# Kernel tuning notes

Measured on AMD Instinct MI355X. Metric: run time of the kernel, lower is better.

Reference implementation:

```python
import jax, jax.numpy as jnp
import numpy as np

B, S, D = 8, 512, 384
VOCAB = 50257


def setup_inputs() -> dict:
    key = jax.random.key(0)
    ks = jax.random.split(key, 8)
    tokens = jax.random.randint(ks[0], (B, S), 0, VOCAB)
    dep_types = jax.random.randint(ks[1], (B, S), 0, 64)
    dep_heads = jax.random.randint(ks[2], (B, S), 0, S)
    tok_table = jax.random.normal(ks[3], (VOCAB, D), dtype=jnp.float32) * 0.02
    # composition bilinear: out[o] = x1 @ Wc[o] @ x2 + bc[o]
    Wc = jax.random.normal(ks[4], (D, D, D), dtype=jnp.float32) * (1.0 / np.sqrt(D))
    bc = jax.random.normal(ks[5], (D,), dtype=jnp.float32) * 0.01
    # reduction Linear(seq_len, 1): weight (1, S), bias (1,)
    Wr = jax.random.normal(ks[6], (1, S), dtype=jnp.float32) * (1.0 / np.sqrt(S))
    br = jax.random.normal(ks[7], (1,), dtype=jnp.float32) * 0.01
    return {"tokens": tokens, "dep_types": dep_types, "dep_heads": dep_heads,
            "tok_table": tok_table, "Wc": Wc, "bc": bc, "Wr": Wr, "br": br}


def _composition_block(tok, heads, Wc, bc, Wr, br):
    # Original math (with the dep_transform-overwrite bug preserved):
    #   dep = tanh(tok)                                   [B,S,D]
    #   expanded[b,s1,s2,:] = tok[b,s2,:]
    #   masked_dep[b,s1,s2,:] = dep[b,s2,:] * (heads[b,s2]==s1)
    #   comp[b,s1,s2,o] = tanh(bilinear(tok[b,s2], masked_dep[b,s1,s2]))[o]
    #   y[b,s1,o] = sum_s2 Wr[0,s2]*comp[b,s1,s2,o] + br[0]
    # Since masked_dep is zero unless heads[b,s2]==s1, bilinear reduces to
    # bias-only (t_off) off-tree and full value (t_on) on-tree -> O(S) scatter.
    dep = jnp.tanh(tok)
    u = jnp.einsum('bsd,ode,bse->bso', tok, Wc, dep)      # [B,S,D] full bilinear value
    t_on = jnp.tanh(u + bc)                               # [B,S,D]
    t_off = jnp.tanh(bc)                                  # [D]
    w = Wr[0]                                             # [S]
    base = t_off * jnp.sum(w) + br[0]                     # [D]
    contrib = (t_on - t_off) * w[None, :, None]           # [B,S,D]
    scat = jax.vmap(lambda h, c: jnp.zeros((S, D), dtype=tok.dtype).at[h].add(c))(heads, contrib)
    return scat + base[None, None, :]                     # [B,S,D]


def reference(tokens, dep_types, dep_heads, tok_table, Wc, bc, Wr, br):
    depth = 1
    tok = tok_table[tokens]                               # [B,S,D]
    # dep_types embedding is computed in the original but its result is
    # discarded inside the block (bug); it does not affect the output.
    for _ in range(depth):
        tok = _composition_block(tok, dep_heads, Wc, bc, Wr, br)
    out_mask = (dep_heads == 0)[:, :, None]               # [B,S,1]
    return tok * out_mask.astype(tok.dtype)
```

## Files before the change

kernel.cpp:

```cpp
#include <hip/hip_runtime.h>

#define BB 8
#define SS 512
#define DD 384
#define K2 (DD * DD)
#define LCH 16
#define OT 4
#define KCH 8
#define NT 256
#define GROUPS (K2 / 4)
#define GPC (GROUPS / KCH)
#define ITERS (GPC / NT)
#define MAXL_CAP 1024

#define WS_LIST_OFF 16
#define WS_U_OFF 16400

__global__ void flag_kernel(const int* __restrict__ heads, int* __restrict__ countp,
                            int* __restrict__ list, int maxl) {
    int b = blockIdx.x;
    int s2 = threadIdx.x;
    int h = heads[b * SS + s2];
    if (heads[b * SS + h] == 0) {
        int idx = atomicAdd(countp, 1);
        if (idx < maxl) list[idx] = b * SS + s2;
    }
}

template <int HALF>
__device__ __forceinline__ void fold_step(float* red, int lane) {
#pragma unroll
    for (int i = 0; i < HALF; ++i) {
        float lo = red[i], hi = red[i + HALF];
        float send = (lane & HALF) ? lo : hi;
        float recv = __shfl_xor(send, HALF, 64);
        red[i] = (lane & HALF) ? (hi + recv) : (lo + recv);
    }
}

__global__ __launch_bounds__(NT, 3) void bilinear_kernel(
    const float* __restrict__ Wc, const float* __restrict__ tok_table,
    const int* __restrict__ tokens, const int* __restrict__ list,
    const int* __restrict__ countp, float* __restrict__ u, int maxl) {
    __shared__ alignas(16) float tokS[LCH][DD];
    __shared__ alignas(16) float depS[LCH][DD];

    const int tid = threadIdx.x;
    const int lane = tid & 63;
    const int wid = tid >> 6;
    const int o0 = blockIdx.x * OT;
    const int g0 = blockIdx.y * GPC;

    int total = *countp;
    if (total > maxl) total = maxl;

    for (int cb = 0; cb < total; cb += LCH) {
        for (int idx = tid; idx < LCH * DD; idx += NT) {
            int l = idx / DD;
            int i = idx - l * DD;
            float t = 0.f;
            if (cb + l < total) {
                int pos = list[cb + l];
                t = tok_table[(size_t)tokens[pos] * DD + i];
            }
            tokS[l][i] = t;
            depS[l][i] = tanhf(t);
        }
        __syncthreads();

        const int lmax = total - cb;

        float acc[LCH][OT];
#pragma unroll
        for (int l = 0; l < LCH; ++l)
#pragma unroll
            for (int j = 0; j < OT; ++j) acc[l][j] = 0.f;

        const float* wbase = Wc + (size_t)o0 * K2;
        float4 wv[OT], nv[OT];
        {
            const float* wp = wbase + 4 * (size_t)(g0 + tid);
#pragma unroll
            for (int r = 0; r < OT; ++r) wv[r] = *(const float4*)(wp + (size_t)r * K2);
        }

#pragma unroll 1
        for (int it = 0; it < ITERS; ++it) {
            int gc = g0 + it * NT + tid;

#pragma unroll
            for (int r = 0; r < OT; ++r) nv[r] = make_float4(0.f, 0.f, 0.f, 0.f);
            if (it + 1 < ITERS) {
                const float* wp = wbase + 4 * (size_t)(gc + NT);
#pragma unroll
                for (int r = 0; r < OT; ++r) nv[r] = *(const float4*)(wp + (size_t)r * K2);
            }

            int d = gc / 96;
            int e4 = gc - d * 96;

#pragma unroll
            for (int l4 = 0; l4 < LCH / 4; ++l4) {
                if (l4 * 4 < lmax) {
#pragma unroll
                    for (int li = 0; li < 4; ++li) {
                        const int l = l4 * 4 + li;
                        float td = tokS[l][d];
                        float4 dv = *(const float4*)(&depS[l][e4 * 4]);
                        float px = td * dv.x, py = td * dv.y;
                        float pz = td * dv.z, pw = td * dv.w;
#pragma unroll
                        for (int r = 0; r < OT; ++r)
                            acc[l][r] += px * wv[r].x + py * wv[r].y +
                                         pz * wv[r].z + pw * wv[r].w;
                    }
                }
            }
#pragma unroll
            for (int r = 0; r < OT; ++r) wv[r] = nv[r];
        }

        float red[LCH * OT];
#pragma unroll
        for (int k = 0; k < LCH * OT; ++k) red[k] = acc[k >> 2][k & 3];
        fold_step<32>(red, lane);
        fold_step<16>(red, lane);
        fold_step<8>(red, lane);
        fold_step<4>(red, lane);
        fold_step<2>(red, lane);
        fold_step<1>(red, lane);

        __syncthreads();
        float* redS = &tokS[0][0];
        redS[wid * 64 + lane] = red[0];
        __syncthreads();
        if (tid < 64) {
            int l = tid >> 2, j = tid & 3;
            if (l < lmax) {
                float s = redS[tid] + redS[64 + tid] + redS[128 + tid] + redS[192 + tid];
                atomicAdd(&u[(size_t)(cb + l) * DD + o0 + j], s);
            }
        }
        __syncthreads();
    }
}

__global__ __launch_bounds__(SS) void finalize_kernel(
    const int* __restrict__ heads, const float* __restrict__ Wr,
    const float* __restrict__ bc, const float* __restrict__ br,
    const int* __restrict__ list, const int* __restrict__ countp,
    const float* __restrict__ u, float* __restrict__ out, int maxl) {
    int b = blockIdx.x;
    int tid = threadIdx.x;

    __shared__ float wpart[SS / 64];
    __shared__ int hitlist[64];
    __shared__ int nh;
    if (tid == 0) nh = 0;
    __syncthreads();

    float w = Wr[tid];
#pragma unroll
    for (int off = 32; off > 0; off >>= 1) w += __shfl_down(w, off, 64);
    if ((tid & 63) == 0) wpart[tid >> 6] = w;

    if (heads[b * SS + tid] == 0) {
        int i = atomicAdd(&nh, 1);
        if (i < 64) hitlist[i] = tid;
    }
    __syncthreads();

    float sumw = 0.f;
#pragma unroll
    for (int q = 0; q < SS / 64; ++q) sumw += wpart[q];
    float brv = br[0];

    int total = *countp;
    if (total > maxl) total = maxl;
    int hn = nh;
    if (hn > 64) hn = 64;

    for (int i = 0; i < hn; ++i) {
        int s1 = hitlist[i];
        if (tid < DD) {
            int o = tid;
            float bco = bc[o];
            float t_off = tanhf(bco);
            float val = t_off * sumw + brv;
            for (int l = 0; l < total; ++l) {
                int pos = list[l];
                if ((pos >> 9) == b && heads[pos] == s1)
                    val += (tanhf(u[(size_t)l * DD + o] + bco) - t_off) * Wr[pos & 511];
            }
            out[(size_t)(b * SS + s1) * DD + o] = val;
        }
    }
}

extern "C" void kernel_launch(void* const* d_in, const int* in_sizes, int n_in,
                              void* d_out, int out_size, void* d_ws, size_t ws_size,
                              hipStream_t stream) {
    const int* tokens = (const int*)d_in[0];
    const int* heads = (const int*)d_in[2];
    const float* tok_table = (const float*)d_in[3];
    const float* Wc = (const float*)d_in[4];
    const float* bc = (const float*)d_in[5];
    const float* Wr = (const float*)d_in[6];
    const float* br = (const float*)d_in[7];
    float* out = (float*)d_out;

    char* ws = (char*)d_ws;
    int* countp = (int*)ws;
    int* list = (int*)(ws + WS_LIST_OFF);
    float* u = (float*)(ws + WS_U_OFF);

    long maxl_l = ((long)ws_size - WS_U_OFF) / (DD * 4);
    int maxl = maxl_l < 0 ? 0 : (maxl_l > MAXL_CAP ? MAXL_CAP : (int)maxl_l);

    hipMemsetAsync(d_ws, 0, (size_t)WS_U_OFF + (size_t)maxl * DD * 4, stream);
    hipMemsetAsync(d_out, 0, (size_t)out_size, stream);

    flag_kernel<<<BB, SS, 0, stream>>>(heads, countp, list, maxl);
    bilinear_kernel<<<dim3(DD / OT, KCH), NT, 0, stream>>>(
        Wc, tok_table, tokens, list, countp, u, maxl);
    finalize_kernel<<<BB, SS, 0, stream>>>(
        heads, Wr, bc, br, list, countp, u, out, maxl);
}
```

Baseline: 373.2 us.

## Precompute gathered token/tanh rows once and replace atomics with per-chunk partials

A single-block prep kernel now builds the list of active positions and writes gathered token embeddings and their tanh into workspace once. The bilinear blocks then only copy these rows with float4 loads instead of each redoing the gather and tanh. The atomic accumulation into u becomes plain stores of per-K-chunk partials, which finalize sums. This also removes the workspace memset and makes the weight prefetch unconditional. The trade-offs are a serial single-block prep stage and more workspace.

```diff
diff --git a/kernel.cpp b/kernel.cpp
--- a/kernel.cpp
+++ b/kernel.cpp
@@ -3,6 +3,7 @@
 #define BB 8
 #define SS 512
 #define DD 384
+#define D4 (DD / 4)
 #define K2 (DD * DD)
 #define LCH 16
 #define OT 4
@@ -12,18 +13,42 @@
 #define GPC (GROUPS / KCH)
 #define ITERS (GPC / NT)
 #define MAXL_CAP 1024
+#define PREP_NT 1024
 
 #define WS_LIST_OFF 16
-#define WS_U_OFF 16400
-
-__global__ void flag_kernel(const int* __restrict__ heads, int* __restrict__ countp,
-                            int* __restrict__ list, int maxl) {
-    int b = blockIdx.x;
-    int s2 = threadIdx.x;
-    int h = heads[b * SS + s2];
-    if (heads[b * SS + h] == 0) {
-        int idx = atomicAdd(countp, 1);
-        if (idx < maxl) list[idx] = b * SS + s2;
+#define WS_TOKW_OFF (WS_LIST_OFF + 4 * MAXL_CAP)
+
+__global__ __launch_bounds__(PREP_NT) void prep_kernel(
+    const int* __restrict__ heads, const int* __restrict__ tokens,
+    const float* __restrict__ tok_table, int* __restrict__ countp,
+    int* __restrict__ list, float* __restrict__ tokW, float* __restrict__ depW,
+    int maxl) {
+    __shared__ int cnt;
+    __shared__ int lst[MAXL_CAP];
+    const int tid = threadIdx.x;
+    if (tid == 0) cnt = 0;
+    __syncthreads();
+
+    for (int pos = tid; pos < BB * SS; pos += PREP_NT) {
+        int h = heads[pos];
+        if (heads[(pos & ~(SS - 1)) + h] == 0) {
+            int i = atomicAdd(&cnt, 1);
+            if (i < maxl) lst[i] = pos;
+        }
+    }
+    __syncthreads();
+
+    int total = cnt;
+    if (total > maxl) total = maxl;
+    if (tid == 0) *countp = total;
+    for (int i = tid; i < total; i += PREP_NT) list[i] = lst[i];
+
+    for (int idx = tid; idx < total * DD; idx += PREP_NT) {
+        int l = idx / DD;
+        int i = idx - l * DD;
+        float t = tok_table[(size_t)tokens[lst[l]] * DD + i];
+        tokW[idx] = t;
+        depW[idx] = tanhf(t);
     }
 }
 
@@ -39,9 +64,9 @@
 }
 
 __global__ __launch_bounds__(NT, 3) void bilinear_kernel(
-    const float* __restrict__ Wc, const float* __restrict__ tok_table,
-    const int* __restrict__ tokens, const int* __restrict__ list,
-    const int* __restrict__ countp, float* __restrict__ u, int maxl) {
+    const float* __restrict__ Wc, const float* __restrict__ tokW,
+    const float* __restrict__ depW, const int* __restrict__ countp,
+    float* __restrict__ u, int maxl) {
     __shared__ alignas(16) float tokS[LCH][DD];
     __shared__ alignas(16) float depS[LCH][DD];
 
@@ -55,16 +80,19 @@
     if (total > maxl) total = maxl;
 
     for (int cb = 0; cb < total; cb += LCH) {
-        for (int idx = tid; idx < LCH * DD; idx += NT) {
-            int l = idx / DD;
-            int i = idx - l * DD;
-            float t = 0.f;
-            if (cb + l < total) {
-                int pos = list[cb + l];
-                t = tok_table[(size_t)tokens[pos] * DD + i];
-            }
-            tokS[l][i] = t;
-            depS[l][i] = tanhf(t);
+        {
+            const float4* tw = (const float4*)tokW;
+            const float4* dw = (const float4*)depW;
+            float4* ts = (float4*)&tokS[0][0];
+            float4* ds = (float4*)&depS[0][0];
+            const float4 z = make_float4(0.f, 0.f, 0.f, 0.f);
+            for (int idx = tid; idx < LCH * D4; idx += NT) {
+                int l = idx / D4;
+                bool live = (cb + l) < total;
+                int src = cb * D4 + idx;
+                ts[idx] = live ? tw[src] : z;
+                ds[idx] = live ? dw[src] : z;
+            }
         }
         __syncthreads();
 
@@ -88,10 +116,9 @@
         for (int it = 0; it < ITERS; ++it) {
             int gc = g0 + it * NT + tid;
 
-#pragma unroll
-            for (int r = 0; r < OT; ++r) nv[r] = make_float4(0.f, 0.f, 0.f, 0.f);
-            if (it + 1 < ITERS) {
-                const float* wp = wbase + 4 * (size_t)(gc + NT);
+            {
+                int gn = (it + 1 < ITERS) ? (gc + NT) : (g0 + tid);
+                const float* wp = wbase + 4 * (size_t)gn;
 #pragma unroll
                 for (int r = 0; r < OT; ++r) nv[r] = *(const float4*)(wp + (size_t)r * K2);
             }
@@ -136,9 +163,9 @@
         __syncthreads();
         if (tid < 64) {
             int l = tid >> 2, j = tid & 3;
-            if (l < lmax) {
+            if (l < lmax && l < LCH) {
                 float s = redS[tid] + redS[64 + tid] + redS[128 + tid] + redS[192 + tid];
-                atomicAdd(&u[(size_t)(cb + l) * DD + o0 + j], s);
+                u[((size_t)blockIdx.y * maxl + (cb + l)) * DD + o0 + j] = s;
             }
         }
         __syncthreads();
@@ -189,8 +216,13 @@
             float val = t_off * sumw + brv;
             for (int l = 0; l < total; ++l) {
                 int pos = list[l];
-                if ((pos >> 9) == b && heads[pos] == s1)
-                    val += (tanhf(u[(size_t)l * DD + o] + bco) - t_off) * Wr[pos & 511];
+                if ((pos >> 9) == b && heads[pos] == s1) {
+                    float sum = 0.f;
+#pragma unroll
+                    for (int c = 0; c < KCH; ++c)
+                        sum += u[((size_t)c * maxl + l) * DD + o];
+                    val += (tanhf(sum + bco) - t_off) * Wr[pos & 511];
+                }
             }
             out[(size_t)(b * SS + s1) * DD + o] = val;
         }
@@ -212,17 +244,22 @@
     char* ws = (char*)d_ws;
     int* countp = (int*)ws;
     int* list = (int*)(ws + WS_LIST_OFF);
-    float* u = (float*)(ws + WS_U_OFF);
-
-    long maxl_l = ((long)ws_size - WS_U_OFF) / (DD * 4);
+
+    long avail = (long)ws_size - WS_TOKW_OFF;
+    long per_row = (long)(2 + KCH) * DD * 4;
+    long maxl_l = avail / per_row;
     int maxl = maxl_l < 0 ? 0 : (maxl_l > MAXL_CAP ? MAXL_CAP : (int)maxl_l);
 
-    hipMemsetAsync(d_ws, 0, (size_t)WS_U_OFF + (size_t)maxl * DD * 4, stream);
+    float* tokW = (float*)(ws + WS_TOKW_OFF);
+    float* depW = tokW + (size_t)maxl * DD;
+    float* u = depW + (size_t)maxl * DD;
+
     hipMemsetAsync(d_out, 0, (size_t)out_size, stream);
 
-    flag_kernel<<<BB, SS, 0, stream>>>(heads, countp, list, maxl);
+    prep_kernel<<<1, PREP_NT, 0, stream>>>(heads, tokens, tok_table,
+                                           countp, list, tokW, depW, maxl);
     bilinear_kernel<<<dim3(DD / OT, KCH), NT, 0, stream>>>(
-        Wc, tok_table, tokens, list, countp, u, maxl);
+        Wc, tokW, depW, countp, u, maxl);
     finalize_kernel<<<BB, SS, 0, stream>>>(
         heads, Wr, bc, br, list, countp, u, out, maxl);
 }
```

Measured after the change: 370.1 us. No clear change (-0.8%).

## Fuse flag list building into bilinear kernel and drop memsets and atomics

Applied to the files above, without the earlier changes.

Every bilinear block now rebuilds the on-tree position list in shared memory with wave ballots, so the separate flag kernel and both memsets go away. Block (0,0) publishes the count and list for the finalize kernel. Per-K-chunk partial sums are written to separate u slices instead of being atomically added, and finalize sums them. Finalize runs one block per output row and zeroes rows that are off the tree directly. In exchange, every block repeats the list construction, the list is capped per wave segment, and the u workspace is KCH times larger.

```diff
diff --git a/kernel.cpp b/kernel.cpp
--- a/kernel.cpp
+++ b/kernel.cpp
@@ -3,6 +3,7 @@
 #define BB 8
 #define SS 512
 #define DD 384
+#define D4 (DD / 4)
 #define K2 (DD * DD)
 #define LCH 16
 #define OT 4
@@ -12,20 +13,10 @@
 #define GPC (GROUPS / KCH)
 #define ITERS (GPC / NT)
 #define MAXL_CAP 1024
+#define SEG_CAP 256
 
 #define WS_LIST_OFF 16
-#define WS_U_OFF 16400
-
-__global__ void flag_kernel(const int* __restrict__ heads, int* __restrict__ countp,
-                            int* __restrict__ list, int maxl) {
-    int b = blockIdx.x;
-    int s2 = threadIdx.x;
-    int h = heads[b * SS + s2];
-    if (heads[b * SS + h] == 0) {
-        int idx = atomicAdd(countp, 1);
-        if (idx < maxl) list[idx] = b * SS + s2;
-    }
-}
+#define WS_U_OFF (WS_LIST_OFF + 4 * MAXL_CAP)
 
 template <int HALF>
 __device__ __forceinline__ void fold_step(float* red, int lane) {
@@ -40,10 +31,13 @@
 
 __global__ __launch_bounds__(NT, 3) void bilinear_kernel(
     const float* __restrict__ Wc, const float* __restrict__ tok_table,
-    const int* __restrict__ tokens, const int* __restrict__ list,
-    const int* __restrict__ countp, float* __restrict__ u, int maxl) {
+    const int* __restrict__ tokens, const int* __restrict__ heads,
+    int* __restrict__ countp, int* __restrict__ list_ws,
+    float* __restrict__ u, int maxl) {
     __shared__ alignas(16) float tokS[LCH][DD];
     __shared__ alignas(16) float depS[LCH][DD];
+    __shared__ int lstS[MAXL_CAP];
+    __shared__ int cw[4];
 
     const int tid = threadIdx.x;
     const int lane = tid & 63;
@@ -51,18 +45,48 @@
     const int o0 = blockIdx.x * OT;
     const int g0 = blockIdx.y * GPC;
 
-    int total = *countp;
+    {
+        int* lstSeg = (int*)&tokS[0][0];
+        int cnt = 0;
+#pragma unroll 4
+        for (int cc = 0; cc < 16; ++cc) {
+            int pos = (wid * 16 + cc) * 64 + lane;
+            int h = heads[pos];
+            bool pred = (heads[(pos & ~(SS - 1)) + h] == 0);
+            unsigned long long m = __ballot(pred);
+            if (pred) {
+                int idx = cnt + __popcll(m & ((1ull << lane) - 1ull));
+                if (idx < SEG_CAP) lstSeg[wid * SEG_CAP + idx] = pos;
+            }
+            cnt += (int)__popcll(m);
+        }
+        if (lane == 0) cw[wid] = cnt > SEG_CAP ? SEG_CAP : cnt;
+        __syncthreads();
+        int offW[4];
+        offW[0] = 0;
+#pragma unroll
+        for (int w = 1; w < 4; ++w) offW[w] = offW[w - 1] + cw[w - 1];
+        for (int i = lane; i < cw[wid]; i += 64) {
+            int dst = offW[wid] + i;
+            if (dst < MAXL_CAP) lstS[dst] = lstSeg[wid * SEG_CAP + i];
+        }
+        __syncthreads();
+    }
+    int total = cw[0] + cw[1] + cw[2] + cw[3];
     if (total > maxl) total = maxl;
+
+    if (blockIdx.x == 0 && blockIdx.y == 0) {
+        if (tid == 0) *countp = total;
+        for (int i = tid; i < total; i += NT) list_ws[i] = lstS[i];
+    }
 
     for (int cb = 0; cb < total; cb += LCH) {
         for (int idx = tid; idx < LCH * DD; idx += NT) {
             int l = idx / DD;
             int i = idx - l * DD;
             float t = 0.f;
-            if (cb + l < total) {
-                int pos = list[cb + l];
-                t = tok_table[(size_t)tokens[pos] * DD + i];
-            }
+            if (cb + l < total)
+                t = tok_table[(size_t)tokens[lstS[cb + l]] * DD + i];
             tokS[l][i] = t;
             depS[l][i] = tanhf(t);
         }
@@ -88,10 +112,9 @@
         for (int it = 0; it < ITERS; ++it) {
             int gc = g0 + it * NT + tid;
 
-#pragma unroll
-            for (int r = 0; r < OT; ++r) nv[r] = make_float4(0.f, 0.f, 0.f, 0.f);
-            if (it + 1 < ITERS) {
-                const float* wp = wbase + 4 * (size_t)(gc + NT);
+            {
+                int gn = (it + 1 < ITERS) ? (gc + NT) : (g0 + tid);
+                const float* wp = wbase + 4 * (size_t)gn;
 #pragma unroll
                 for (int r = 0; r < OT; ++r) nv[r] = *(const float4*)(wp + (size_t)r * K2);
             }
@@ -136,64 +159,58 @@
         __syncthreads();
         if (tid < 64) {
             int l = tid >> 2, j = tid & 3;
-            if (l < lmax) {
+            if (l < lmax && l < LCH) {
                 float s = redS[tid] + redS[64 + tid] + redS[128 + tid] + redS[192 + tid];
-                atomicAdd(&u[(size_t)(cb + l) * DD + o0 + j], s);
-            }
-        }
-        __syncthreads();
-    }
-}
-
-__global__ __launch_bounds__(SS) void finalize_kernel(
+                u[((size_t)blockIdx.y * maxl + (cb + l)) * DD + o0 + j] = s;
+            }
+        }
+        __syncthreads();
+    }
+}
+
+__global__ __launch_bounds__(128) void finalize_kernel(
     const int* __restrict__ heads, const float* __restrict__ Wr,
     const float* __restrict__ bc, const float* __restrict__ br,
     const int* __restrict__ list, const int* __restrict__ countp,
     const float* __restrict__ u, float* __restrict__ out, int maxl) {
-    int b = blockIdx.x;
+    int row = blockIdx.x;
     int tid = threadIdx.x;
 
-    __shared__ float wpart[SS / 64];
-    __shared__ int hitlist[64];
-    __shared__ int nh;
-    if (tid == 0) nh = 0;
+    if (heads[row] != 0) {
+        if (tid < D4)
+            ((float4*)(out + (size_t)row * DD))[tid] = make_float4(0.f, 0.f, 0.f, 0.f);
+        return;
+    }
+    int b = row >> 9;
+    int s1 = row & 511;
+
+    __shared__ float wsum[2];
+    float w = Wr[tid] + Wr[tid + 128] + Wr[tid + 256] + Wr[tid + 384];
+#pragma unroll
+    for (int off = 32; off > 0; off >>= 1) w += __shfl_down(w, off, 64);
+    if ((tid & 63) == 0) wsum[tid >> 6] = w;
     __syncthreads();
-
-    float w = Wr[tid];
-#pragma unroll
-    for (int off = 32; off > 0; off >>= 1) w += __shfl_down(w, off, 64);
-    if ((tid & 63) == 0) wpart[tid >> 6] = w;
-
-    if (heads[b * SS + tid] == 0) {
-        int i = atomicAdd(&nh, 1);
-        if (i < 64) hitlist[i] = tid;
-    }
-    __syncthreads();
-
-    float sumw = 0.f;
-#pragma unroll
-    for (int q = 0; q < SS / 64; ++q) sumw += wpart[q];
+    float sumw = wsum[0] + wsum[1];
     float brv = br[0];
 
     int total = *countp;
     if (total > maxl) total = maxl;
-    int hn = nh;
-    if (hn > 64) hn = 64;
-
-    for (int i = 0; i < hn; ++i) {
-        int s1 = hitlist[i];
-        if (tid < DD) {
-            int o = tid;
-            float bco = bc[o];
-            float t_off = tanhf(bco);
-            float val = t_off * sumw + brv;
-            for (int l = 0; l < total; ++l) {
-                int pos = list[l];
-                if ((pos >> 9) == b && heads[pos] == s1)
-                    val += (tanhf(u[(size_t)l * DD + o] + bco) - t_off) * Wr[pos & 511];
-            }
-            out[(size_t)(b * SS + s1) * DD + o] = val;
-        }
+
+    for (int o = tid; o < DD; o += 128) {
+        float bco = bc[o];
+        float t_off = tanhf(bco);
+        float val = t_off * sumw + brv;
+        for (int l = 0; l < total; ++l) {
+            int pos = list[l];
+            if ((pos >> 9) == b && heads[pos] == s1) {
+                float sum = 0.f;
+#pragma unroll
+                for (int c = 0; c < KCH; ++c)
+                    sum += u[((size_t)c * maxl + l) * DD + o];
+                val += (tanhf(sum + bco) - t_off) * Wr[pos & 511];
+            }
+        }
+        out[(size_t)row * DD + o] = val;
     }
 }
 
@@ -212,17 +229,16 @@
     char* ws = (char*)d_ws;
     int* countp = (int*)ws;
     int* list = (int*)(ws + WS_LIST_OFF);
+
+    long avail = (long)ws_size - WS_U_OFF;
+    long per_row = (long)KCH * DD * 4;
+    long maxl_l = avail / per_row;
+    int maxl = maxl_l < 0 ? 0 : (maxl_l > MAXL_CAP ? MAXL_CAP : (int)maxl_l);
+
     float* u = (float*)(ws + WS_U_OFF);
 
-    long maxl_l = ((long)ws_size - WS_U_OFF) / (DD * 4);
-    int maxl = maxl_l < 0 ? 0 : (maxl_l > MAXL_CAP ? MAXL_CAP : (int)maxl_l);
-
-    hipMemsetAsync(d_ws, 0, (size_t)WS_U_OFF + (size_t)maxl * DD * 4, stream);
-    hipMemsetAsync(d_out, 0, (size_t)out_size, stream);
-
-    flag_kernel<<<BB, SS, 0, stream>>>(heads, countp, list, maxl);
     bilinear_kernel<<<dim3(DD / OT, KCH), NT, 0, stream>>>(
-        Wc, tok_table, tokens, list, countp, u, maxl);
-    finalize_kernel<<<BB, SS, 0, stream>>>(
+        Wc, tok_table, tokens, heads, countp, list, u, maxl);
+    finalize_kernel<<<BB * SS, 128, 0, stream>>>(
         heads, Wr, bc, br, list, countp, u, out, maxl);
 }
```

Result: no change. 375.1 us (+0.5%).
